# Optimization experiments

Hardware: AMD Instinct MI355X
Metric: run time of the kernel (lower is better)

## Reference

```python
import jax, jax.numpy as jnp
import numpy as np


def setup_inputs() -> dict:
    key = jax.random.key(0)
    k1, k2, k3 = jax.random.split(key, 3)
    N = 100000
    E = 1600000
    d = 128
    indices = jax.random.randint(k1, (2, E), 0, N, dtype=jnp.int64)
    values = jax.random.uniform(k2, (E,), dtype=jnp.float32)
    b = jax.random.normal(k3, (N, d), dtype=jnp.float32)
    return {"indices": indices, "values": values, "b": b, "N": N, "layer_id": 0}


def reference(indices, values, b, N, layer_id):
    # Sparse COO matmul: out[r] = sum_{e: row[e]==r} values[e] * b[col[e]]
    row = indices[0]  # [E]
    col = indices[1]  # [E]
    contrib = values[:, None] * b[col]  # [E, d] gathered + scaled edge messages
    out = jax.ops.segment_sum(contrib, row, num_segments=N)  # [N, d]
    return out
```

## Files before the change

kernel.cpp:

```cpp
#include <hip/hip_runtime.h>


#define DIM 128
#define RPB 32
#define BLK 128
#define STAGE 768
#define CAP (STAGE + 7 * RPB)
#define NCH1 2048
#define PB2 8
#define MAXNB 4096
#define MAXNSB 128
#define OVFCAP 16384

__device__ __forceinline__ unsigned short f2bf(float f) {
    unsigned u = __float_as_uint(f);
    return (unsigned short)((u + 0x7FFFu + ((u >> 16) & 1u)) >> 16);
}
__device__ __forceinline__ float4 ldbf4(const char* p) {
    ushort4 h = *reinterpret_cast<const ushort4*>(p);
    float4 r;
    r.x = __uint_as_float((unsigned)h.x << 16);
    r.y = __uint_as_float((unsigned)h.y << 16);
    r.z = __uint_as_float((unsigned)h.z << 16);
    r.w = __uint_as_float((unsigned)h.w << 16);
    return r;
}

__global__ __launch_bounds__(256) void spmm_atomic_kernel(
    const int* __restrict__ rows, const int* __restrict__ cols,
    const float* __restrict__ vals, const float* __restrict__ b,
    float* __restrict__ out, int E)
{
    long long t = (long long)blockIdx.x * blockDim.x + threadIdx.x;
    int e = (int)(t >> 5);
    if (e >= E) return;
    int j = ((int)t & 31) * 4;
    int r = rows[e]; int c = cols[e]; float v = vals[e];
    const float4 bv = *reinterpret_cast<const float4*>(b + (size_t)c * DIM + j);
    float* o = out + (size_t)r * DIM + j;
    atomicAdd(o + 0, v * bv.x);
    atomicAdd(o + 1, v * bv.y);
    atomicAdd(o + 2, v * bv.z);
    atomicAdd(o + 3, v * bv.w);
}

#define PACK(VAL, COL, ROW)                                                  \
    (((unsigned long long)(unsigned)__float_as_int(VAL) << 32) |             \
     (unsigned)(((COL) << 10) | ((ROW) & 1023)))

__global__ __launch_bounds__(256) void p1fix_kernel(
    const int* __restrict__ rows, const int* __restrict__ cols,
    const float* __restrict__ vals, int* __restrict__ scnt, int SCAP,
    unsigned long long* __restrict__ pairs1, int E,
    const float* __restrict__ b, unsigned short* __restrict__ bh, int n4,
    int* __restrict__ ovfn, unsigned long long* __restrict__ ovfpc,
    int* __restrict__ ovfrow)
{
    {
        const float4* b4 = reinterpret_cast<const float4*>(b);
        ushort4* bh4 = reinterpret_cast<ushort4*>(bh);
        const int stride = gridDim.x * 256;
        int i = blockIdx.x * 256 + threadIdx.x;
        for (; i + 3 * stride < n4; i += 4 * stride) {
            float4 v0 = b4[i];
            float4 v1 = b4[i + stride];
            float4 v2 = b4[i + 2 * stride];
            float4 v3 = b4[i + 3 * stride];
            ushort4 h0 = {f2bf(v0.x), f2bf(v0.y), f2bf(v0.z), f2bf(v0.w)};
            ushort4 h1 = {f2bf(v1.x), f2bf(v1.y), f2bf(v1.z), f2bf(v1.w)};
            ushort4 h2 = {f2bf(v2.x), f2bf(v2.y), f2bf(v2.z), f2bf(v2.w)};
            ushort4 h3 = {f2bf(v3.x), f2bf(v3.y), f2bf(v3.z), f2bf(v3.w)};
            bh4[i] = h0;
            bh4[i + stride] = h1;
            bh4[i + 2 * stride] = h2;
            bh4[i + 3 * stride] = h3;
        }
        for (; i < n4; i += stride) {
            float4 v = b4[i];
            ushort4 h = {f2bf(v.x), f2bf(v.y), f2bf(v.z), f2bf(v.w)};
            bh4[i] = h;
        }
    }

    __shared__ int hist[MAXNSB];
    __shared__ int base[MAXNSB];
    if (threadIdx.x < MAXNSB) hist[threadIdx.x] = 0;
    __syncthreads();
    const int chunk = (E + NCH1 - 1) / NCH1;
    const int s = blockIdx.x * chunk;
    const int e = min(s + chunk, E);
    const int t = threadIdx.x;

    {
        int i = s + t;
        for (; i + 768 < e; i += 1024) {
            int r0 = rows[i], r1 = rows[i + 256];
            int r2 = rows[i + 512], r3 = rows[i + 768];
            atomicAdd(&hist[r0 >> 10], 1);
            atomicAdd(&hist[r1 >> 10], 1);
            atomicAdd(&hist[r2 >> 10], 1);
            atomicAdd(&hist[r3 >> 10], 1);
        }
        for (; i < e; i += 256) atomicAdd(&hist[rows[i] >> 10], 1);
    }
    __syncthreads();
    if (threadIdx.x < MAXNSB) {
        int c = hist[threadIdx.x];
        base[threadIdx.x] = c ? atomicAdd(&scnt[threadIdx.x], c) : 0;
        hist[threadIdx.x] = 0;
    }
    __syncthreads();

#define SCATTER1(R, C, V)                                                    \
    {                                                                        \
        int sb = (R) >> 10;                                                  \
        int rel = base[sb] + atomicAdd(&hist[sb], 1);                        \
        if (rel < SCAP) {                                                    \
            pairs1[(size_t)sb * SCAP + rel] = PACK(V, C, R);                 \
        } else {                                                             \
            int slot = atomicAdd(ovfn, 1);                                   \
            if (slot < OVFCAP) {                                             \
                ovfpc[slot] = ((unsigned long long)(unsigned)                \
                               __float_as_int(V) << 32) | (unsigned)(C);     \
                ovfrow[slot] = (R);                                          \
            }                                                                \
        }                                                                    \
    }

    {
        int i = s + t;
        for (; i + 768 < e; i += 1024) {
            int   r0 = rows[i],     r1 = rows[i + 256];
            int   r2 = rows[i + 512], r3 = rows[i + 768];
            int   c0 = cols[i],     c1 = cols[i + 256];
            int   c2 = cols[i + 512], c3 = cols[i + 768];
            float v0 = vals[i],     v1 = vals[i + 256];
            float v2 = vals[i + 512], v3 = vals[i + 768];
            SCATTER1(r0, c0, v0) SCATTER1(r1, c1, v1)
            SCATTER1(r2, c2, v2) SCATTER1(r3, c3, v3)
        }
        for (; i < e; i += 256) {
            int r = rows[i]; int c = cols[i]; float v = vals[i];
            SCATTER1(r, c, v)
        }
    }
#undef SCATTER1
}

__global__ __launch_bounds__(256) void p2fix_kernel(
    const int* __restrict__ scnt, int SCAP, int* __restrict__ bcnt, int BCAP,
    const unsigned long long* __restrict__ pairs1,
    unsigned long long* __restrict__ pairs2, int NB,
    int* __restrict__ ovfn, unsigned long long* __restrict__ ovfpc,
    int* __restrict__ ovfrow)
{
    int sb = blockIdx.x / PB2;
    int q  = blockIdx.x % PB2;
    int b0 = sb * 32;
    int len = min(scnt[sb], SCAP);
    size_t sbase = (size_t)sb * SCAP;
    int s = (int)((long long)len * q / PB2);
    int e = (int)((long long)len * (q + 1) / PB2);

    __shared__ int hist[32];
    __shared__ int base[32];
    if (threadIdx.x < 32) hist[threadIdx.x] = 0;
    __syncthreads();
    for (int i = s + threadIdx.x; i < e; i += 256)
        atomicAdd(&hist[((unsigned)pairs1[sbase + i] >> 5) & 31], 1);
    __syncthreads();
    if (threadIdx.x < 32) {
        int c = hist[threadIdx.x];
        int cb = b0 + threadIdx.x;
        base[threadIdx.x] = (c && cb < NB) ? atomicAdd(&bcnt[cb], c) : 0;
        hist[threadIdx.x] = 0;
    }
    __syncthreads();
    for (int i = s + threadIdx.x; i < e; i += 256) {
        unsigned long long p = pairs1[sbase + i];
        unsigned lo = (unsigned)p;
        int sub = (lo >> 5) & 31;
        int rel = base[sub] + atomicAdd(&hist[sub], 1);
        if (rel < BCAP) {
            pairs2[(size_t)(b0 + sub) * BCAP + rel] = p;
        } else {
            int slot = atomicAdd(ovfn, 1);
            if (slot < OVFCAP) {
                ovfpc[slot] = (p & 0xffffffff00000000ull) | (lo >> 10);
                ovfrow[slot] = sb * 1024 + (int)(lo & 1023u);
            }
        }
    }
}

__global__ __launch_bounds__(256) void fixup_kernel(
    const int* __restrict__ ovfn, const unsigned long long* __restrict__ ovfpc,
    const int* __restrict__ ovfrow, const unsigned short* __restrict__ bh,
    float* __restrict__ out)
{
    int n = min(*ovfn, OVFCAP);
    int g = threadIdx.x >> 5, lane = threadIdx.x & 31;
    for (int i = g; i < n; i += 8) {
        unsigned long long p = ovfpc[i];
        float v = __int_as_float((int)(p >> 32));
        int col = (int)(unsigned)(p & 0xffffffffu);
        int row = ovfrow[i];
        float4 bv = ldbf4((const char*)bh + (size_t)col * 256 + lane * 8);
        float* o = out + (size_t)row * DIM + lane * 4;
        atomicAdd(o + 0, v * bv.x);
        atomicAdd(o + 1, v * bv.y);
        atomicAdd(o + 2, v * bv.z);
        atomicAdd(o + 3, v * bv.w);
    }
}

__global__ __launch_bounds__(BLK) void bucket_accum_kernel(
    const int* __restrict__ bcnt, int BCAP,
    const unsigned long long* __restrict__ pairs,
    const unsigned short* __restrict__ bmat, float* __restrict__ out, int N)
{
    __shared__ int2 svec[CAP];
    __shared__ int fcnt[RPB];
    __shared__ int foff[RPB + 1];
    __shared__ int stmp[RPB];

    int cb = blockIdx.x;
    size_t cstart = (size_t)cb * BCAP;
    int Mtot = min(bcnt[cb], BCAP);
    int M = min(Mtot, STAGE);
    int t = threadIdx.x;

    unsigned long long ep0 = 0, ep1 = 0, ep2 = 0, ep3 = 0, ep4 = 0, ep5 = 0;
    {
        const unsigned long long* p = pairs + cstart;
        if (t         < M) ep0 = p[t];
        if (t + 128   < M) ep1 = p[t + 128];
        if (t + 256   < M) ep2 = p[t + 256];
        if (t + 384   < M) ep3 = p[t + 384];
        if (t + 512   < M) ep4 = p[t + 512];
        if (t + 640   < M) ep5 = p[t + 640];
    }
    for (int i = t; i < CAP; i += BLK) svec[i] = make_int2(0, 0);
    if (t < RPB) fcnt[t] = 0;
    __syncthreads();

    if (t         < M) atomicAdd(&fcnt[(int)(ep0 & 31u)], 1);
    if (t + 128   < M) atomicAdd(&fcnt[(int)(ep1 & 31u)], 1);
    if (t + 256   < M) atomicAdd(&fcnt[(int)(ep2 & 31u)], 1);
    if (t + 384   < M) atomicAdd(&fcnt[(int)(ep3 & 31u)], 1);
    if (t + 512   < M) atomicAdd(&fcnt[(int)(ep4 & 31u)], 1);
    if (t + 640   < M) atomicAdd(&fcnt[(int)(ep5 & 31u)], 1);
    __syncthreads();

    int pc = 0;
    if (t < RPB) { pc = (fcnt[t] + 7) & ~7; stmp[t] = pc; }
    __syncthreads();
    for (int off = 1; off < RPB; off <<= 1) {
        int x = 0;
        if (t < RPB && t >= off) x = stmp[t - off];
        __syncthreads();
        if (t < RPB) stmp[t] += x;
        __syncthreads();
    }
    if (t < RPB) {
        int excl = stmp[t] - pc;
        foff[t] = excl;
        fcnt[t] = excl;
    }
    if (t == RPB - 1) foff[RPB] = stmp[t];
    __syncthreads();

#define RANK_WRITE(EP, OFS)                                                  \
    if (t + (OFS) < M) {                                                     \
        unsigned lo = (unsigned)(EP & 0xffffffffu);                          \
        int pos = atomicAdd(&fcnt[(int)(lo & 31u)], 1);                      \
        svec[pos] = make_int2((int)((lo >> 10) << 8), (int)(EP >> 32));      \
    }
    RANK_WRITE(ep0, 0)   RANK_WRITE(ep1, 128) RANK_WRITE(ep2, 256)
    RANK_WRITE(ep3, 384) RANK_WRITE(ep4, 512) RANK_WRITE(ep5, 640)
#undef RANK_WRITE
    __syncthreads();

    int wid  = t >> 6;
    int lane = t & 63;
    int h    = lane >> 5;
    int sub  = lane & 31;
    const char* blh = (const char*)bmat + sub * 8;

#define FMA4(EV, CV)                                                         \
    { float v = __int_as_float(EV.y);                                        \
      acc.x = fmaf(v, CV.x, acc.x); acc.y = fmaf(v, CV.y, acc.y);            \
      acc.z = fmaf(v, CV.z, acc.z); acc.w = fmaf(v, CV.w, acc.w); }

    for (int j = 0; j < 16; ++j) {
        int rl = wid * 16 + j;
        int rg = cb * RPB + rl;
        if (rg >= N) break;
        float4 acc = make_float4(0.f, 0.f, 0.f, 0.f);
        int ks = foff[rl], ke = foff[rl + 1];
        if (ks < ke) {
            int2 e0 = svec[ks + h],     e1 = svec[ks + 2 + h];
            int2 e2 = svec[ks + 4 + h], e3 = svec[ks + 6 + h];
            float4 c0 = ldbf4(blh + e0.x);
            float4 c1 = ldbf4(blh + e1.x);
            float4 c2 = ldbf4(blh + e2.x);
            float4 c3 = ldbf4(blh + e3.x);
            for (int k = ks + 8; k < ke; k += 8) {
                int2 f0 = svec[k + h],     f1 = svec[k + 2 + h];
                int2 f2 = svec[k + 4 + h], f3 = svec[k + 6 + h];
                float4 d0 = ldbf4(blh + f0.x);
                float4 d1 = ldbf4(blh + f1.x);
                float4 d2 = ldbf4(blh + f2.x);
                float4 d3 = ldbf4(blh + f3.x);
                __builtin_amdgcn_sched_barrier(0);
                FMA4(e0, c0) FMA4(e1, c1) FMA4(e2, c2) FMA4(e3, c3)
                e0 = f0; e1 = f1; e2 = f2; e3 = f3;
                c0 = d0; c1 = d1; c2 = d2; c3 = d3;
            }
            FMA4(e0, c0) FMA4(e1, c1) FMA4(e2, c2) FMA4(e3, c3)
        }
        if (h == 0) {
            for (int q = STAGE; q < Mtot; ++q) {
                unsigned long long p = pairs[cstart + q];
                if ((int)(p & 31u) == rl) {
                    unsigned lo = (unsigned)(p & 0xffffffffu);
                    float v = __int_as_float((int)(p >> 32));
                    float4 bv = ldbf4(blh + (int)((lo >> 10) << 8));
                    acc.x = fmaf(v, bv.x, acc.x); acc.y = fmaf(v, bv.y, acc.y);
                    acc.z = fmaf(v, bv.z, acc.z); acc.w = fmaf(v, bv.w, acc.w);
                }
            }
        }
        acc.x += __shfl_xor(acc.x, 32);
        acc.y += __shfl_xor(acc.y, 32);
        acc.z += __shfl_xor(acc.z, 32);
        acc.w += __shfl_xor(acc.w, 32);
        if (h == 0)
            *reinterpret_cast<float4*>(out + (size_t)rg * DIM + sub * 4) = acc;
    }
#undef FMA4
}

extern "C" void kernel_launch(void* const* d_in, const int* in_sizes, int n_in,
                              void* d_out, int out_size, void* d_ws, size_t ws_size,
                              hipStream_t stream)
{
    const int*   indices = (const int*)d_in[0];
    const float* vals    = (const float*)d_in[1];
    const float* b       = (const float*)d_in[2];
    float*       out     = (float*)d_out;

    const int E = in_sizes[1];
    const int N = in_sizes[2] / DIM;
    const int* rows = indices;
    const int* cols = indices + E;

    const int NB  = (N + RPB - 1) / RPB;
    const int NSB = (NB + 31) / 32;

    const int SCAP = E / NSB + 1024;
    const int BCAP = E / NB + 128;
    size_t bh_bytes  = (size_t)N * DIM * 2;
    size_t p1f_bytes = (size_t)NSB * SCAP * 8;
    size_t p2f_bytes = (size_t)NB * BCAP * 8;
    size_t ctr_bytes = (size_t)(NSB + NB + 2) * 4;
    size_t ovf_bytes = (size_t)OVFCAP * 12;
    size_t needed_fix = p2f_bytes + bh_bytes + p1f_bytes + ctr_bytes + ovf_bytes;

    if (ws_size < needed_fix || NB > MAXNB || NB < 1 || E < 1 || N > (1 << 17)) {
        hipMemsetAsync(d_out, 0, (size_t)out_size * sizeof(float), stream);
        if (E >= 1) {
            const long long total = (long long)E * 32;
            const int grid = (int)((total + 255) / 256);
            spmm_atomic_kernel<<<grid, 256, 0, stream>>>(rows, cols, vals, b, out, E);
        }
        return;
    }

    char* base = (char*)d_ws;
    unsigned long long* pairs2 = (unsigned long long*)base;
    size_t off = p2f_bytes;
    unsigned short* bh = (unsigned short*)(base + off); off += bh_bytes;
    unsigned long long* pairs1 = (unsigned long long*)(base + off); off += p1f_bytes;
    int* scnt = (int*)(base + off);
    int* bcnt = scnt + NSB;
    int* ovfn = bcnt + NB;
    off += ctr_bytes;
    unsigned long long* ovfpc = (unsigned long long*)(base + off);
    int* ovfrow = (int*)(ovfpc + OVFCAP);

    const int n4 = N * DIM / 4;
    hipMemsetAsync(scnt, 0, ctr_bytes, stream);
    p1fix_kernel<<<NCH1, 256, 0, stream>>>(
        rows, cols, vals, scnt, SCAP, pairs1, E, b, bh, n4,
        ovfn, ovfpc, ovfrow);
    p2fix_kernel<<<NSB * PB2, 256, 0, stream>>>(
        scnt, SCAP, bcnt, BCAP, pairs1, pairs2, NB, ovfn, ovfpc, ovfrow);
    bucket_accum_kernel<<<NB, BLK, 0, stream>>>(
        bcnt, BCAP, pairs2, bh, out, N);
    fixup_kernel<<<1, 256, 0, stream>>>(ovfn, ovfpc, ovfrow, bh, out);
}
```

Baseline: 156.6 us.

## Locally sort edges by super-bucket in shared memory before coalesced scatter

The first partition pass now loads each block's chunk of edges into registers once. It builds a super-bucket histogram and runs a shared-memory prefix scan, then ranks the packed entries into a shared buffer grouped by super-bucket. It then writes them to global memory in contiguous runs, instead of scattering each edge directly with per-edge atomics. The block count is halved so each block handles up to 1792 edges, and a fallback guard covers larger chunks. This adds more barriers and shared memory in exchange for more coalesced global writes and a single read of the inputs.

Result: faster. 131.3 us (-16.1%).

```diff
diff --git a/kernel.cpp b/kernel.cpp
--- a/kernel.cpp
+++ b/kernel.cpp
@@ -6,7 +6,8 @@
 #define BLK 128
 #define STAGE 768
 #define CAP (STAGE + 7 * RPB)
-#define NCH1 2048
+#define NCH1 1024
+#define EPB 1792
 #define PB2 8
 #define MAXNB 4096
 #define MAXNSB 128
@@ -48,7 +49,7 @@
     (((unsigned long long)(unsigned)__float_as_int(VAL) << 32) |             \
      (unsigned)(((COL) << 10) | ((ROW) & 1023)))
 
-__global__ __launch_bounds__(256) void p1fix_kernel(
+__global__ __launch_bounds__(256) void p1sort_kernel(
     const int* __restrict__ rows, const int* __restrict__ cols,
     const float* __restrict__ vals, int* __restrict__ scnt, int SCAP,
     unsigned long long* __restrict__ pairs1, int E,
@@ -56,95 +57,98 @@
     int* __restrict__ ovfn, unsigned long long* __restrict__ ovfpc,
     int* __restrict__ ovfrow)
 {
-    {
-        const float4* b4 = reinterpret_cast<const float4*>(b);
-        ushort4* bh4 = reinterpret_cast<ushort4*>(bh);
-        const int stride = gridDim.x * 256;
-        int i = blockIdx.x * 256 + threadIdx.x;
-        for (; i + 3 * stride < n4; i += 4 * stride) {
-            float4 v0 = b4[i];
-            float4 v1 = b4[i + stride];
-            float4 v2 = b4[i + 2 * stride];
-            float4 v3 = b4[i + 3 * stride];
-            ushort4 h0 = {f2bf(v0.x), f2bf(v0.y), f2bf(v0.z), f2bf(v0.w)};
-            ushort4 h1 = {f2bf(v1.x), f2bf(v1.y), f2bf(v1.z), f2bf(v1.w)};
-            ushort4 h2 = {f2bf(v2.x), f2bf(v2.y), f2bf(v2.z), f2bf(v2.w)};
-            ushort4 h3 = {f2bf(v3.x), f2bf(v3.y), f2bf(v3.z), f2bf(v3.w)};
-            bh4[i] = h0;
-            bh4[i + stride] = h1;
-            bh4[i + 2 * stride] = h2;
-            bh4[i + 3 * stride] = h3;
-        }
-        for (; i < n4; i += stride) {
-            float4 v = b4[i];
-            ushort4 h = {f2bf(v.x), f2bf(v.y), f2bf(v.z), f2bf(v.w)};
-            bh4[i] = h;
-        }
-    }
-
+    for (int i = blockIdx.x * blockDim.x + threadIdx.x; i < n4;
+         i += gridDim.x * blockDim.x) {
+        float4 v = reinterpret_cast<const float4*>(b)[i];
+        ushort4 h = {f2bf(v.x), f2bf(v.y), f2bf(v.z), f2bf(v.w)};
+        reinterpret_cast<ushort4*>(bh)[i] = h;
+    }
+
+    __shared__ unsigned long long svec[EPB];
+    __shared__ unsigned char      sbof[EPB];
     __shared__ int hist[MAXNSB];
-    __shared__ int base[MAXNSB];
-    if (threadIdx.x < MAXNSB) hist[threadIdx.x] = 0;
-    __syncthreads();
+    __shared__ int foff[MAXNSB];
+    __shared__ int gbase[MAXNSB];
+    __shared__ int stmp[MAXNSB];
+
     const int chunk = (E + NCH1 - 1) / NCH1;
     const int s = blockIdx.x * chunk;
     const int e = min(s + chunk, E);
+    const int cnt = e - s;
     const int t = threadIdx.x;
 
+    int   r0 = 0, r1 = 0, r2 = 0, r3 = 0, r4 = 0, r5 = 0, r6 = 0;
+    int   c0 = 0, c1 = 0, c2 = 0, c3 = 0, c4 = 0, c5 = 0, c6 = 0;
+    float v0 = 0, v1 = 0, v2 = 0, v3 = 0, v4 = 0, v5 = 0, v6 = 0;
     {
-        int i = s + t;
-        for (; i + 768 < e; i += 1024) {
-            int r0 = rows[i], r1 = rows[i + 256];
-            int r2 = rows[i + 512], r3 = rows[i + 768];
-            atomicAdd(&hist[r0 >> 10], 1);
-            atomicAdd(&hist[r1 >> 10], 1);
-            atomicAdd(&hist[r2 >> 10], 1);
-            atomicAdd(&hist[r3 >> 10], 1);
+        const int* rp = rows + s; const int* cp = cols + s;
+        const float* vp = vals + s;
+        if (t          < cnt) { r0 = rp[t];        c0 = cp[t];        v0 = vp[t]; }
+        if (t +  256   < cnt) { r1 = rp[t + 256];  c1 = cp[t + 256];  v1 = vp[t + 256]; }
+        if (t +  512   < cnt) { r2 = rp[t + 512];  c2 = cp[t + 512];  v2 = vp[t + 512]; }
+        if (t +  768   < cnt) { r3 = rp[t + 768];  c3 = cp[t + 768];  v3 = vp[t + 768]; }
+        if (t + 1024   < cnt) { r4 = rp[t + 1024]; c4 = cp[t + 1024]; v4 = vp[t + 1024]; }
+        if (t + 1280   < cnt) { r5 = rp[t + 1280]; c5 = cp[t + 1280]; v5 = vp[t + 1280]; }
+        if (t + 1536   < cnt) { r6 = rp[t + 1536]; c6 = cp[t + 1536]; v6 = vp[t + 1536]; }
+    }
+    if (t < MAXNSB) hist[t] = 0;
+    __syncthreads();
+
+    if (t          < cnt) atomicAdd(&hist[r0 >> 10], 1);
+    if (t +  256   < cnt) atomicAdd(&hist[r1 >> 10], 1);
+    if (t +  512   < cnt) atomicAdd(&hist[r2 >> 10], 1);
+    if (t +  768   < cnt) atomicAdd(&hist[r3 >> 10], 1);
+    if (t + 1024   < cnt) atomicAdd(&hist[r4 >> 10], 1);
+    if (t + 1280   < cnt) atomicAdd(&hist[r5 >> 10], 1);
+    if (t + 1536   < cnt) atomicAdd(&hist[r6 >> 10], 1);
+    __syncthreads();
+
+    int hv = 0;
+    if (t < MAXNSB) { hv = hist[t]; stmp[t] = hv; }
+    __syncthreads();
+    for (int off = 1; off < MAXNSB; off <<= 1) {
+        int x = 0;
+        if (t < MAXNSB && t >= off) x = stmp[t - off];
+        __syncthreads();
+        if (t < MAXNSB) stmp[t] += x;
+        __syncthreads();
+    }
+    if (t < MAXNSB) {
+        int excl = stmp[t] - hv;
+        foff[t] = excl;
+        hist[t] = excl;
+        gbase[t] = hv ? atomicAdd(&scnt[t], hv) : 0;
+    }
+    __syncthreads();
+
+#define RANKW(R, C, V, OFS)                                                  \
+    if (t + (OFS) < cnt) {                                                   \
+        int sb = (R) >> 10;                                                  \
+        int pos = atomicAdd(&hist[sb], 1);                                   \
+        svec[pos] = PACK(V, C, R);                                           \
+        sbof[pos] = (unsigned char)sb;                                       \
+    }
+    RANKW(r0, c0, v0, 0)    RANKW(r1, c1, v1, 256)  RANKW(r2, c2, v2, 512)
+    RANKW(r3, c3, v3, 768)  RANKW(r4, c4, v4, 1024) RANKW(r5, c5, v5, 1280)
+    RANKW(r6, c6, v6, 1536)
+#undef RANKW
+    __syncthreads();
+
+    for (int i = t; i < cnt; i += 256) {
+        int sb = sbof[i];
+        unsigned long long p = svec[i];
+        int rel = gbase[sb] + (i - foff[sb]);
+        if (rel < SCAP) {
+            pairs1[(size_t)sb * SCAP + rel] = p;
+        } else {
+            int slot = atomicAdd(ovfn, 1);
+            if (slot < OVFCAP) {
+                unsigned lo = (unsigned)p;
+                ovfpc[slot] = (p & 0xffffffff00000000ull) | (lo >> 10);
+                ovfrow[slot] = sb * 1024 + (int)(lo & 1023u);
+            }
         }
-        for (; i < e; i += 256) atomicAdd(&hist[rows[i] >> 10], 1);
-    }
-    __syncthreads();
-    if (threadIdx.x < MAXNSB) {
-        int c = hist[threadIdx.x];
-        base[threadIdx.x] = c ? atomicAdd(&scnt[threadIdx.x], c) : 0;
-        hist[threadIdx.x] = 0;
-    }
-    __syncthreads();
-
-#define SCATTER1(R, C, V)                                                    \
-    {                                                                        \
-        int sb = (R) >> 10;                                                  \
-        int rel = base[sb] + atomicAdd(&hist[sb], 1);                        \
-        if (rel < SCAP) {                                                    \
-            pairs1[(size_t)sb * SCAP + rel] = PACK(V, C, R);                 \
-        } else {                                                             \
-            int slot = atomicAdd(ovfn, 1);                                   \
-            if (slot < OVFCAP) {                                             \
-                ovfpc[slot] = ((unsigned long long)(unsigned)                \
-                               __float_as_int(V) << 32) | (unsigned)(C);     \
-                ovfrow[slot] = (R);                                          \
-            }                                                                \
-        }                                                                    \
-    }
-
-    {
-        int i = s + t;
-        for (; i + 768 < e; i += 1024) {
-            int   r0 = rows[i],     r1 = rows[i + 256];
-            int   r2 = rows[i + 512], r3 = rows[i + 768];
-            int   c0 = cols[i],     c1 = cols[i + 256];
-            int   c2 = cols[i + 512], c3 = cols[i + 768];
-            float v0 = vals[i],     v1 = vals[i + 256];
-            float v2 = vals[i + 512], v3 = vals[i + 768];
-            SCATTER1(r0, c0, v0) SCATTER1(r1, c1, v1)
-            SCATTER1(r2, c2, v2) SCATTER1(r3, c3, v3)
-        }
-        for (; i < e; i += 256) {
-            int r = rows[i]; int c = cols[i]; float v = vals[i];
-            SCATTER1(r, c, v)
-        }
-    }
-#undef SCATTER1
+    }
 }
 
 __global__ __launch_bounds__(256) void p2fix_kernel(
@@ -367,7 +371,10 @@
     size_t ovf_bytes = (size_t)OVFCAP * 12;
     size_t needed_fix = p2f_bytes + bh_bytes + p1f_bytes + ctr_bytes + ovf_bytes;
 
-    if (ws_size < needed_fix || NB > MAXNB || NB < 1 || E < 1 || N > (1 << 17)) {
+    const int chunk = (E + NCH1 - 1) / NCH1;
+
+    if (ws_size < needed_fix || NB > MAXNB || NB < 1 || E < 1 ||
+        N > (1 << 17) || chunk > EPB) {
         hipMemsetAsync(d_out, 0, (size_t)out_size * sizeof(float), stream);
         if (E >= 1) {
             const long long total = (long long)E * 32;
@@ -391,7 +398,7 @@
 
     const int n4 = N * DIM / 4;
     hipMemsetAsync(scnt, 0, ctr_bytes, stream);
-    p1fix_kernel<<<NCH1, 256, 0, stream>>>(
+    p1sort_kernel<<<NCH1, 256, 0, stream>>>(
         rows, cols, vals, scnt, SCAP, pairs1, E, b, bh, n4,
         ovfn, ovfpc, ovfrow);
     p2fix_kernel<<<NSB * PB2, 256, 0, stream>>>(
```
